# Optimization experiments

Hardware: AMD Instinct MI355X
Metric: run time of the kernel (lower is better)

## Reference

```python
import jax, jax.numpy as jnp
import numpy as np

N = 50000
E = 800000
D = 64


def _linear_params(key, d, bias=True):
    kw, kb = jax.random.split(key)
    s = 1.0 / np.sqrt(d)
    W = jax.random.uniform(kw, (d, d), jnp.float32, -s, s)
    if bias:
        b = jax.random.uniform(kb, (d,), jnp.float32, -s, s)
        return W, b
    return W


def setup_inputs() -> dict:
    key = jax.random.key(0)
    ks = jax.random.split(key, 12)
    x_src = jax.random.normal(ks[0], (N, D), jnp.float32)
    x_tgt = jax.random.normal(ks[1], (N, D), jnp.float32)
    t_src = jax.random.normal(ks[2], (N, D), jnp.float32)
    t_tgt = jax.random.normal(ks[3], (N, D), jnp.float32)
    edge_index = jax.random.randint(ks[4], (2, E), 0, N, jnp.int64)
    W_x = _linear_params(ks[5], D, bias=False)
    W_t = _linear_params(ks[6], D, bias=False)
    Ka_W, Ka_b = _linear_params(ks[7], D)
    Qa_W, Qa_b = _linear_params(ks[8], D)
    Kb_W, Kb_b = _linear_params(ks[9], D)
    Qb_W, Qb_b = _linear_params(ks[10], D)
    return dict(x_src=x_src, x_tgt=x_tgt, t_src=t_src, t_tgt=t_tgt,
                edge_index=edge_index, W_x=W_x, W_t=W_t,
                Ka_W=Ka_W, Ka_b=Ka_b, Qa_W=Qa_W, Qa_b=Qa_b,
                Kb_W=Kb_W, Kb_b=Kb_b, Qb_W=Qb_W, Qb_b=Qb_b)


def _segment_softmax(scores, seg, num_segments):
    # numerically stable softmax over edges sharing the same destination node
    m = jax.ops.segment_max(scores, seg, num_segments=num_segments)
    ex = jnp.exp(scores - m[seg])
    denom = jax.ops.segment_sum(ex, seg, num_segments=num_segments)
    return ex / denom[seg]


def reference(x_src, x_tgt, t_src, t_tgt, edge_index,
              W_x, W_t, Ka_W, Ka_b, Qa_W, Qa_b, Kb_W, Kb_b, Qb_W, Qb_b):
    row, col = edge_index[0], edge_index[1]
    n = x_tgt.shape[0]
    d = x_src.shape[-1]
    scale = 1.0 / jnp.sqrt(jnp.float32(d))

    # project on nodes first (cheaper than per-edge), then gather per edge
    q_alpha = (t_tgt @ Qa_W.T + Qa_b)[row]   # [E, D]
    k_alpha = (t_src @ Ka_W.T + Ka_b)[col]
    alpha = _segment_softmax(jnp.sum(q_alpha * k_alpha, -1) * scale, row, n)

    q_beta = (x_tgt @ Qb_W.T + Qb_b)[row]
    k_beta = (x_src @ Kb_W.T + Kb_b)[col]
    beta = _segment_softmax(jnp.sum(q_beta * k_beta, -1) * scale, row, n)

    msg_t = alpha[:, None] * (t_src @ W_t.T)[col]  # [E, D]
    msg_x = beta[:, None] * (x_src @ W_x.T)[col]

    out_x = jax.ops.segment_sum(msg_x, row, num_segments=n)
    out_t = jax.ops.segment_sum(msg_t, row, num_segments=n)
    return out_x, out_t
```

## Files before the change

### kernel.cpp

```cpp
#include <hip/hip_runtime.h>
#include <math.h>


#define D 64
#define NINF -3.0e38f
typedef unsigned short ushortT;
typedef unsigned long long ull;
typedef __attribute__((ext_vector_type(8))) short bf16x8;
typedef __attribute__((ext_vector_type(4))) float f32x4;

__device__ __forceinline__ float b2f_lo(unsigned u) {
  return __uint_as_float(u << 16);
}
__device__ __forceinline__ float b2f_hi(unsigned u) {
  return __uint_as_float(u & 0xffff0000u);
}
__device__ __forceinline__ ushortT f2b(float f) {
  unsigned u = __float_as_uint(f);
  u += 0x7fffu + ((u >> 16) & 1u);
  return (ushortT)(u >> 16);
}
__device__ __forceinline__ bf16x8 pack8(float4 v0, float4 v1) {
  bf16x8 r;
  r[0] = (short)f2b(v0.x); r[1] = (short)f2b(v0.y);
  r[2] = (short)f2b(v0.z); r[3] = (short)f2b(v0.w);
  r[4] = (short)f2b(v1.x); r[5] = (short)f2b(v1.y);
  r[6] = (short)f2b(v1.z); r[7] = (short)f2b(v1.w);
  return r;
}

__device__ __forceinline__ bool wave_is64(const ull* __restrict__ ei, ull nNodes) {
  ull v = ei[threadIdx.x & 63];
  return __ballot(v >= nNodes) == 0ull;
}

__global__ __launch_bounds__(256) void scat_proj(
    const void* __restrict__ ei, int* __restrict__ degp,
    int* __restrict__ ecol, int CAP, int E,
    const float* __restrict__ t_tgt, const float* __restrict__ x_tgt,
    const float* __restrict__ t_src, const float* __restrict__ x_src,
    const float* __restrict__ QaW, const float* __restrict__ Qab_,
    const float* __restrict__ QbW, const float* __restrict__ Qbb,
    const float* __restrict__ KaW, const float* __restrict__ Kab_,
    const float* __restrict__ Wt,
    const float* __restrict__ KbW, const float* __restrict__ Kbb,
    const float* __restrict__ Wx,
    float* __restrict__ qab, ushortT* __restrict__ kab, ushortT* __restrict__ vtx,
    int N, int bpj, int scatBlocks) {
  const int tid = threadIdx.x;

  if (blockIdx.x < scatBlocks) {
    const bool is64 = wave_is64((const ull*)ei, (ull)N);
    int base = (blockIdx.x * 256 + tid) << 2;
    if (base >= E) return;
    int m = E - base; if (m > 4) m = 4;
    if (is64) {
      const long long* p = (const long long*)ei;
      for (int j = 0; j < m; ++j) {
        int r = (int)p[base + j];
        int c = (int)p[(long long)E + base + j];
        int rk = atomicAdd(&degp[(size_t)r << 4], 1);
        if (rk < CAP) ecol[(size_t)r * CAP + rk] = c;
      }
    } else {
      const int* p = (const int*)ei;
      for (int j = 0; j < m; ++j) {
        int r = p[base + j];
        int c = p[E + base + j];
        int rk = atomicAdd(&degp[(size_t)r << 4], 1);
        if (rk < CAP) ecol[(size_t)r * CAP + rk] = c;
      }
    }
    return;
  }

  const int tile = blockIdx.x - scatBlocks;
  const int job = tile / bpj;
  const int jb = tile % bpj;
  const float *X, *W0, *B0, *W1 = nullptr;
  switch (job) {
    case 0: X = t_tgt; W0 = QaW; B0 = Qab_; break;
    case 1: X = x_tgt; W0 = QbW; B0 = Qbb; break;
    case 2: X = t_src; W0 = KaW; B0 = Kab_; W1 = Wt; break;
    default: X = x_src; W0 = KbW; B0 = Kbb; W1 = Wx; break;
  }
  const bool dual = (job >= 2);
  const int half = (job & 1) ? 64 : 0;
  const int base = jb * 128;

  const int lane = tid & 63;
  const int wid = tid >> 6;
  const int m16 = lane & 15;
  const int quad = lane >> 4;

  f32x4 acc0[2][4], acc1[2][4];
#pragma unroll
  for (int mt = 0; mt < 2; ++mt)
#pragma unroll
    for (int nt = 0; nt < 4; ++nt) {
      acc0[mt][nt] = (f32x4){0.f, 0.f, 0.f, 0.f};
      acc1[mt][nt] = (f32x4){0.f, 0.f, 0.f, 0.f};
    }

#pragma unroll
  for (int ko = 0; ko < 2; ++ko) {
    const int koff = ko * 32 + quad * 8;
    bf16x8 a[2];
#pragma unroll
    for (int mt = 0; mt < 2; ++mt) {
      const int gnode = base + wid * 32 + mt * 16 + m16;
      float4 v0 = make_float4(0.f, 0.f, 0.f, 0.f), v1 = v0;
      if (gnode < N) {
        const float* p = X + (size_t)gnode * D + koff;
        v0 = *(const float4*)p;
        v1 = *(const float4*)(p + 4);
      }
      a[mt] = pack8(v0, v1);
    }
#pragma unroll
    for (int nt = 0; nt < 4; ++nt) {
      const float* pw = W0 + (nt * 16 + m16) * D + koff;
      bf16x8 b = pack8(*(const float4*)pw, *(const float4*)(pw + 4));
#pragma unroll
      for (int mt = 0; mt < 2; ++mt)
        acc0[mt][nt] = __builtin_amdgcn_mfma_f32_16x16x32_bf16(
            a[mt], b, acc0[mt][nt], 0, 0, 0);
    }
    if (dual) {
#pragma unroll
      for (int nt = 0; nt < 4; ++nt) {
        const float* pw = W1 + (nt * 16 + m16) * D + koff;
        bf16x8 b = pack8(*(const float4*)pw, *(const float4*)(pw + 4));
#pragma unroll
        for (int mt = 0; mt < 2; ++mt)
          acc1[mt][nt] = __builtin_amdgcn_mfma_f32_16x16x32_bf16(
              a[mt], b, acc1[mt][nt], 0, 0, 0);
      }
    }
  }

  float bias[4];
#pragma unroll
  for (int nt = 0; nt < 4; ++nt) bias[nt] = B0[nt * 16 + m16];
#pragma unroll
  for (int mt = 0; mt < 2; ++mt) {
#pragma unroll
    for (int reg = 0; reg < 4; ++reg) {
      int node = base + wid * 32 + mt * 16 + quad * 4 + reg;
      if (node < N) {
        if (!dual) {
          float* dst = qab + (size_t)node * 128 + half;
#pragma unroll
          for (int nt = 0; nt < 4; ++nt)
            dst[nt * 16 + m16] = acc0[mt][nt][reg] + bias[nt];
        } else {
          ushortT* dk = kab + (size_t)node * 128 + half;
          ushortT* dv = vtx + (size_t)node * 128 + half;
#pragma unroll
          for (int nt = 0; nt < 4; ++nt) {
            dk[nt * 16 + m16] = f2b(acc0[mt][nt][reg] + bias[nt]);
            dv[nt * 16 + m16] = f2b(acc1[mt][nt][reg]);
          }
        }
      }
    }
  }
}

__global__ __launch_bounds__(256) void node_attn(
    const float* __restrict__ qab, const ushortT* __restrict__ kab,
    const ushortT* __restrict__ vtx,
    const int* __restrict__ degp, const int* __restrict__ ecol, int CAP,
    float* __restrict__ out_x, float* __restrict__ out_t, int nNodes) {
  const int lane = threadIdx.x & 63;
  const int sub = lane >> 4;
  const int sl = lane & 15;
  const int gw = (blockIdx.x * blockDim.x + threadIdx.x) >> 6;
  const int nw = (gridDim.x * blockDim.x) >> 6;
  const float scale = 0.125f;

  for (int n = gw; n < nNodes; n += nw) {
    int dg = degp[(size_t)n << 4];
    if (dg > CAP) dg = CAP;
    const size_t nb = (size_t)n * D;
    if (dg == 0) {
      out_t[nb + lane] = 0.f;
      out_x[nb + lane] = 0.f;
      continue;
    }
    const size_t s = (size_t)n * CAP;
    const float4 q0 = *(const float4*)(qab + (size_t)n * 128 + sl * 8);
    const float4 q1 = *(const float4*)(qab + (size_t)n * 128 + sl * 8 + 4);

    float m = NINF, d = 0.f;
    float acc[8];
#pragma unroll
    for (int j = 0; j < 8; ++j) acc[j] = 0.f;

    for (int i = 0; i < dg; i += 16) {
      int cc[4];
      bool av[4];
#pragma unroll
      for (int j = 0; j < 4; ++j) {
        int ix = i + j * 4 + sub;
        av[j] = ix < dg;
        cc[j] = ecol[s + (av[j] ? ix : 0)];
      }
      uint4 kv[4], vv[4];
#pragma unroll
      for (int j = 0; j < 4; ++j) {
        const ull co = ((ull)(unsigned)cc[j] << 8) + ((unsigned)sl << 4);
        kv[j] = *(const uint4*)((const char*)kab + co);
        vv[j] = *(const uint4*)((const char*)vtx + co);
      }
#pragma unroll
      for (int j = 0; j < 4; ++j) {
        float t = q0.x * b2f_lo(kv[j].x);
        t = fmaf(q0.y, b2f_hi(kv[j].x), t);
        t = fmaf(q0.z, b2f_lo(kv[j].y), t);
        t = fmaf(q0.w, b2f_hi(kv[j].y), t);
        t = fmaf(q1.x, b2f_lo(kv[j].z), t);
        t = fmaf(q1.y, b2f_hi(kv[j].z), t);
        t = fmaf(q1.z, b2f_lo(kv[j].w), t);
        t = fmaf(q1.w, b2f_hi(kv[j].w), t);
#pragma unroll
        for (int off = 1; off < 8; off <<= 1) t += __shfl_xor(t, off);
        const float sc = av[j] ? t * scale : NINF;
        const float mN = fmaxf(m, sc);
        const float f = __expf(m - mN);
        const float w = av[j] ? __expf(sc - mN) : 0.f;
        d = d * f + w;
        acc[0] = fmaf(acc[0], f, w * b2f_lo(vv[j].x));
        acc[1] = fmaf(acc[1], f, w * b2f_hi(vv[j].x));
        acc[2] = fmaf(acc[2], f, w * b2f_lo(vv[j].y));
        acc[3] = fmaf(acc[3], f, w * b2f_hi(vv[j].y));
        acc[4] = fmaf(acc[4], f, w * b2f_lo(vv[j].z));
        acc[5] = fmaf(acc[5], f, w * b2f_hi(vv[j].z));
        acc[6] = fmaf(acc[6], f, w * b2f_lo(vv[j].w));
        acc[7] = fmaf(acc[7], f, w * b2f_hi(vv[j].w));
        m = mN;
      }
    }

    float mg = m;
#pragma unroll
    for (int off = 16; off < 64; off <<= 1) mg = fmaxf(mg, __shfl_xor(mg, off));
    const float fg = __expf(m - mg);
    d *= fg;
#pragma unroll
    for (int j = 0; j < 8; ++j) acc[j] *= fg;
#pragma unroll
    for (int off = 16; off < 64; off <<= 1) {
      d += __shfl_xor(d, off);
#pragma unroll
      for (int j = 0; j < 8; ++j) acc[j] += __shfl_xor(acc[j], off);
    }
    const float inv = 1.0f / d;
    if (sub == 0) {
      float4 o0, o1;
      o0.x = acc[0] * inv; o0.y = acc[1] * inv;
      o0.z = acc[2] * inv; o0.w = acc[3] * inv;
      o1.x = acc[4] * inv; o1.y = acc[5] * inv;
      o1.z = acc[6] * inv; o1.w = acc[7] * inv;
      float* dst = (sl < 8) ? (out_t + nb + sl * 8) : (out_x + nb + (sl - 8) * 8);
      *(float4*)dst = o0;
      *(float4*)(dst + 4) = o1;
    }
  }
}

extern "C" void kernel_launch(void* const* d_in, const int* in_sizes, int n_in,
                              void* d_out, int out_size, void* d_ws, size_t ws_size,
                              hipStream_t stream) {
  const float* x_src = (const float*)d_in[0];
  const float* x_tgt = (const float*)d_in[1];
  const float* t_src = (const float*)d_in[2];
  const float* t_tgt = (const float*)d_in[3];
  const void* edge_index = d_in[4];
  const float* W_x = (const float*)d_in[5];
  const float* W_t = (const float*)d_in[6];
  const float* Ka_W = (const float*)d_in[7];
  const float* Ka_b = (const float*)d_in[8];
  const float* Qa_W = (const float*)d_in[9];
  const float* Qa_b = (const float*)d_in[10];
  const float* Kb_W = (const float*)d_in[11];
  const float* Kb_b = (const float*)d_in[12];
  const float* Qb_W = (const float*)d_in[13];
  const float* Qb_b = (const float*)d_in[14];

  const int N = in_sizes[0] / D;
  const int E = in_sizes[4] / 2;

  char* ws = (char*)d_ws;
  size_t ofs = 0;
  auto carve = [&](size_t bytes) {
    size_t p = ofs;
    ofs += (bytes + 255) & ~(size_t)255;
    return p;
  };
  float* qab = (float*)(ws + carve((size_t)N * 128 * 4));
  ushortT* kab = (ushortT*)(ws + carve((size_t)N * 128 * 2));
  ushortT* vtx = (ushortT*)(ws + carve((size_t)N * 128 * 2));
  int* degp = (int*)(ws + carve((size_t)N * 64));
  size_t avail = (ws_size > ofs) ? (ws_size - ofs) : 0;
  int CAP = (int)(avail / ((size_t)N * 4));
  if (CAP > 128) CAP = 128;
  if (CAP < 64) CAP = 64;
  int* ecol = (int*)(ws + carve((size_t)N * CAP * 4));

  float* out_x = (float*)d_out;
  float* out_t = out_x + (size_t)N * D;

  const int scatBlocks = ((E + 3) / 4 + 255) / 256;
  const int bpj = (N + 127) / 128;

  hipMemsetAsync(degp, 0, (size_t)N * 64, stream);
  scat_proj<<<scatBlocks + 4 * bpj, 256, 0, stream>>>(
      edge_index, degp, ecol, CAP, E,
      t_tgt, x_tgt, t_src, x_src,
      Qa_W, Qa_b, Qb_W, Qb_b,
      Ka_W, Ka_b, W_t,
      Kb_W, Kb_b, W_x,
      qab, kab, vtx, N, bpj, scatBlocks);
  node_attn<<<(N + 3) / 4, 256, 0, stream>>>(qab, kab, vtx, degp, ecol, CAP,
                                             out_x, out_t, N);
}
```

Before: 261.8 us.

## Split scatter and projection into separate kernels, batch 8 atomics per thread

Separates the fused scatter/projection kernel into a dedicated edge-bucketing kernel and a projection kernel launched one after the other. The scatter kernel now handles 8 edges per thread, with all loads, atomics and stores unrolled into separate phases, so more atomics are in flight at once. This gives up the overlap of the scatter and GEMM blocks inside one launch and adds an extra kernel launch, in return for simpler kernels and more memory-level parallelism on the atomics.

```diff
diff --git a/kernel.cpp b/kernel.cpp
--- a/kernel.cpp
+++ b/kernel.cpp
@@ -34,9 +34,62 @@
   return __ballot(v >= nNodes) == 0ull;
 }
 
-__global__ __launch_bounds__(256) void scat_proj(
+__global__ __launch_bounds__(256) void scat(
     const void* __restrict__ ei, int* __restrict__ degp,
-    int* __restrict__ ecol, int CAP, int E,
+    int* __restrict__ ecol, int CAP, int E, int N) {
+  const bool is64 = wave_is64((const ull*)ei, (ull)N);
+  const int gid = blockIdx.x * 256 + threadIdx.x;
+  const int base = gid << 3;
+  if (base >= E) return;
+  const int m = (E - base) < 8 ? (E - base) : 8;
+
+  int r[8], c[8], rk[8];
+  if (is64) {
+    const long long* p = (const long long*)ei;
+    if (m == 8) {
+#pragma unroll
+      for (int j = 0; j < 8; ++j) {
+        r[j] = (int)p[base + j];
+        c[j] = (int)p[(long long)E + base + j];
+      }
+#pragma unroll
+      for (int j = 0; j < 8; ++j) rk[j] = atomicAdd(&degp[(size_t)r[j] << 4], 1);
+#pragma unroll
+      for (int j = 0; j < 8; ++j)
+        if (rk[j] < CAP) ecol[(size_t)r[j] * CAP + rk[j]] = c[j];
+    } else {
+      for (int j = 0; j < m; ++j) {
+        int rr = (int)p[base + j];
+        int cc = (int)p[(long long)E + base + j];
+        int k = atomicAdd(&degp[(size_t)rr << 4], 1);
+        if (k < CAP) ecol[(size_t)rr * CAP + k] = cc;
+      }
+    }
+  } else {
+    const int* p = (const int*)ei;
+    if (m == 8) {
+#pragma unroll
+      for (int j = 0; j < 8; ++j) {
+        r[j] = p[base + j];
+        c[j] = p[E + base + j];
+      }
+#pragma unroll
+      for (int j = 0; j < 8; ++j) rk[j] = atomicAdd(&degp[(size_t)r[j] << 4], 1);
+#pragma unroll
+      for (int j = 0; j < 8; ++j)
+        if (rk[j] < CAP) ecol[(size_t)r[j] * CAP + rk[j]] = c[j];
+    } else {
+      for (int j = 0; j < m; ++j) {
+        int rr = p[base + j];
+        int cc = p[E + base + j];
+        int k = atomicAdd(&degp[(size_t)rr << 4], 1);
+        if (k < CAP) ecol[(size_t)rr * CAP + k] = cc;
+      }
+    }
+  }
+}
+
+__global__ __launch_bounds__(256) void proj(
     const float* __restrict__ t_tgt, const float* __restrict__ x_tgt,
     const float* __restrict__ t_src, const float* __restrict__ x_src,
     const float* __restrict__ QaW, const float* __restrict__ Qab_,
@@ -46,35 +99,9 @@
     const float* __restrict__ KbW, const float* __restrict__ Kbb,
     const float* __restrict__ Wx,
     float* __restrict__ qab, ushortT* __restrict__ kab, ushortT* __restrict__ vtx,
-    int N, int bpj, int scatBlocks) {
+    int N, int bpj) {
   const int tid = threadIdx.x;
-
-  if (blockIdx.x < scatBlocks) {
-    const bool is64 = wave_is64((const ull*)ei, (ull)N);
-    int base = (blockIdx.x * 256 + tid) << 2;
-    if (base >= E) return;
-    int m = E - base; if (m > 4) m = 4;
-    if (is64) {
-      const long long* p = (const long long*)ei;
-      for (int j = 0; j < m; ++j) {
-        int r = (int)p[base + j];
-        int c = (int)p[(long long)E + base + j];
-        int rk = atomicAdd(&degp[(size_t)r << 4], 1);
-        if (rk < CAP) ecol[(size_t)r * CAP + rk] = c;
-      }
-    } else {
-      const int* p = (const int*)ei;
-      for (int j = 0; j < m; ++j) {
-        int r = p[base + j];
-        int c = p[E + base + j];
-        int rk = atomicAdd(&degp[(size_t)r << 4], 1);
-        if (rk < CAP) ecol[(size_t)r * CAP + rk] = c;
-      }
-    }
-    return;
-  }
-
-  const int tile = blockIdx.x - scatBlocks;
+  const int tile = blockIdx.x;
   const int job = tile / bpj;
   const int jb = tile % bpj;
   const float *X, *W0, *B0, *W1 = nullptr;
@@ -311,17 +338,17 @@
   float* out_x = (float*)d_out;
   float* out_t = out_x + (size_t)N * D;
 
-  const int scatBlocks = ((E + 3) / 4 + 255) / 256;
+  const int scatGrid = (E + 8 * 256 - 1) / (8 * 256);
   const int bpj = (N + 127) / 128;
 
   hipMemsetAsync(degp, 0, (size_t)N * 64, stream);
-  scat_proj<<<scatBlocks + 4 * bpj, 256, 0, stream>>>(
-      edge_index, degp, ecol, CAP, E,
+  scat<<<scatGrid, 256, 0, stream>>>(edge_index, degp, ecol, CAP, E, N);
+  proj<<<4 * bpj, 256, 0, stream>>>(
       t_tgt, x_tgt, t_src, x_src,
       Qa_W, Qa_b, Qb_W, Qb_b,
       Ka_W, Ka_b, W_t,
       Kb_W, Kb_b, W_x,
-      qab, kab, vtx, N, bpj, scatBlocks);
+      qab, kab, vtx, N, bpj);
   node_attn<<<(N + 3) / 4, 256, 0, stream>>>(qab, kab, vtx, degp, ecol, CAP,
                                              out_x, out_t, N);
 }
```

Measured after the change: 245.0 us. -6.4%, faster.
